# Kernel optimization log

Hardware: AMD Instinct MI355X
Metric: run time of the kernel (lower is better)

Reference implementation:

```python
import jax, jax.numpy as jnp
import numpy as np

K_MASK = -2.3819763e+38
BLOCK_SIZE = 16  # vLLM default paged-KV block size


def apply_rope(inputs, positions, head_dim, max_wavelength=10000):
    # inputs: [B, T, n, H]; positions: [B, T]
    fraction = 2 * jnp.arange(0, head_dim // 2) / head_dim
    timescale = max_wavelength ** fraction
    sinusoid = positions[..., None] / timescale[None, None, :]  # [B, T, H/2]
    sinusoid = sinusoid[..., None, :]                           # [B, T, 1, H/2]
    sin, cos = jnp.sin(sinusoid), jnp.cos(sinusoid)
    first, second = jnp.split(inputs, 2, axis=-1)
    out = jnp.concatenate([first * cos - second * sin,
                           second * cos + first * sin], axis=-1)
    return out.astype(inputs.dtype)


def write_to_cache(proj, cache_side, slot_mapping):
    # proj: [B, T, K, H]; cache_side: [num_slots, K, H]; slot_mapping: [B, T]
    B, T, K, H = proj.shape
    return cache_side.at[slot_mapping.reshape(-1)].set(proj.reshape(B * T, K, H))


def paged_attn(q, k_cache, v_cache, block_tables, context_lens, sm_scale):
    # q: [B, T=1, N, H]; k_cache/v_cache: [num_slots, Kv, H]
    B, T, N, H = q.shape
    Kv = k_cache.shape[1]
    G = N // Kv  # GQA group size
    nb = block_tables.shape[1]
    L = nb * BLOCK_SIZE
    # flat slot indices for every (possibly padded) position of each sequence
    slots = (block_tables[:, :, None] * BLOCK_SIZE
             + jnp.arange(BLOCK_SIZE)[None, None, :]).reshape(B, L)
    keys = k_cache[slots]  # [B, L, Kv, H] gather over non-contiguous blocks
    vals = v_cache[slots]
    qg = q.reshape(B, T, Kv, G, H) * sm_scale
    logits = jnp.einsum('btkgh,blkh->btkgl', qg, keys)
    valid = jnp.arange(L)[None, :] < context_lens[:, None]  # [B, L]
    logits = jnp.where(valid[:, None, None, None, :], logits, K_MASK)
    probs = jax.nn.softmax(logits, axis=-1).astype(keys.dtype)
    out = jnp.einsum('btkgl,blkh->btkgh', probs, vals)
    return out.reshape(B, T, N, H)


def setup_inputs() -> dict:
    key = jax.random.key(0)
    ks = jax.random.split(key, 8)
    B, D, N, Kv, H = 64, 4096, 32, 8, 128
    blocks_per_seq = 64
    num_blocks = B * blocks_per_seq
    num_slots = num_blocks * BLOCK_SIZE  # 65536

    x = jax.random.normal(ks[0], (B, 1, D), jnp.float32)
    context_lens = jax.random.randint(
        ks[1], (B,), 512, blocks_per_seq * BLOCK_SIZE + 1).astype(jnp.int32)
    segment_pos = (context_lens - 1)[:, None].astype(jnp.int32)  # current token pos
    # disjoint block tables: a permutation of all blocks
    block_tables = jax.random.permutation(ks[2], num_blocks).reshape(
        B, blocks_per_seq).astype(jnp.int32)
    last = context_lens - 1
    slot_mapping = (block_tables[jnp.arange(B), last // BLOCK_SIZE] * BLOCK_SIZE
                    + last % BLOCK_SIZE)[:, None].astype(jnp.int32)
    cache = jax.random.normal(ks[3], (2, num_slots, Kv, H), jnp.float32) * 0.02
    q_w = jax.random.normal(ks[4], (N, D, H), jnp.float32) * 0.02
    kv_w = jax.random.normal(ks[5], (2, Kv, D, H), jnp.float32) * 0.02
    o_w = jax.random.normal(ks[6], (N, H, D), jnp.float32) * 0.02
    return dict(x=x, segment_pos=segment_pos, slot_mapping=slot_mapping,
                block_tables=block_tables, context_lens=context_lens,
                cache=cache, q_w=q_w, kv_w=kv_w, o_w=o_w)


def reference(x, segment_pos, slot_mapping, block_tables, context_lens,
              cache, q_w, kv_w, o_w):
    head_dim = q_w.shape[-1]
    sm_scale = head_dim ** (-0.5)
    # GQA projections (num_kv_heads != num_heads path)
    query = jnp.einsum('BTD,NDH->BTNH', x, q_w)
    key_p, val_p = jnp.einsum('BSD,CKDH->CBSKH', x, kv_w)
    query = apply_rope(query, segment_pos, head_dim)
    key_p = apply_rope(key_p, segment_pos, head_dim)
    # scatter-write new K/V into paged cache
    k_cache = write_to_cache(key_p, cache[0], slot_mapping)
    v_cache = write_to_cache(val_p, cache[1], slot_mapping)
    new_cache = jnp.stack([k_cache, v_cache])
    # paged attention over non-contiguous blocks
    out = paged_attn(query, k_cache, v_cache, block_tables, context_lens, sm_scale)
    attn_output = jnp.einsum('BTNH,NHD->BTD', out, o_w)
    return (new_cache, attn_output)
```

## Files before the change

kernel.cpp:

```cpp
#include <hip/hip_runtime.h>
#include <math.h>

#define BB     64
#define DD     4096
#define NQ     32
#define KVH    8
#define GG     4
#define HD     128
#define PAGES  64
#define PSIZE  16
#define NSLOTS 65536
#define CACHE1 67108864UL
#define CACHE2 134217728UL
#define ATTN_ELEMS (BB*DD)
#define K_MASK_F (-2.3819763e+38f)
#define SM_SCALE 0.08838834764831845f

#define WS_QKV 0UL
#define WS_QR  393216UL
#define WS_AT  655360UL
#define WS_KV  917504UL
#define WS_KV_V 65536UL

__global__ __launch_bounds__(256) void kz_zero(float4* __restrict__ ws,
                                               float4* __restrict__ out) {
    const int i = blockIdx.x * 256 + threadIdx.x;
    if (i < 98304) {
        ws[i] = float4{0.f, 0.f, 0.f, 0.f};
    } else {
        out[CACHE2 / 4 + (i - 98304)] = float4{0.f, 0.f, 0.f, 0.f};
    }
}

__global__ __launch_bounds__(256) void k2_qkv(const float* __restrict__ x,
                                              const float* __restrict__ q_w,
                                              const float* __restrict__ kv_w,
                                              float* __restrict__ ws_qkv) {
    const int jt = blockIdx.x;
    const int u  = blockIdx.y;
    const float* w = (u < 32) ? (q_w + (size_t)u * DD * HD)
                              : (kv_w + (size_t)(u - 32) * DD * HD);
    const int t  = threadIdx.x;
    const int dc = t & 31;
    const int bh = t >> 5;

    __shared__ float lx[64][128];
    float acc[8][4];
    #pragma unroll
    for (int i = 0; i < 8; ++i)
        #pragma unroll
        for (int d = 0; d < 4; ++d) acc[i][d] = 0.f;

    for (int chunk = 0; chunk < 4; ++chunk) {
        const int jc = jt * 512 + chunk * 128;
        __syncthreads();
        const float4* x4 = reinterpret_cast<const float4*>(x);
        float4* lx4 = reinterpret_cast<float4*>(&lx[0][0]);
        for (int f = t; f < 64 * 32; f += 256) {
            int i = f >> 5, j4 = f & 31;
            lx4[i * 32 + j4] = x4[(size_t)i * (DD / 4) + (jc / 4) + j4];
        }
        __syncthreads();

        const float* wp = w + (size_t)jc * HD + dc;
        for (int jj4 = 0; jj4 < 32; ++jj4) {
            float wv[4][4];
            #pragma unroll
            for (int q = 0; q < 4; ++q)
                #pragma unroll
                for (int d = 0; d < 4; ++d)
                    wv[q][d] = wp[(size_t)(jj4 * 4 + q) * HD + d * 32];
            #pragma unroll
            for (int i = 0; i < 8; ++i) {
                float4 xv = *reinterpret_cast<const float4*>(&lx[bh * 8 + i][jj4 * 4]);
                #pragma unroll
                for (int d = 0; d < 4; ++d)
                    acc[i][d] += xv.x * wv[0][d] + xv.y * wv[1][d] +
                                 xv.z * wv[2][d] + xv.w * wv[3][d];
            }
        }
    }
    #pragma unroll
    for (int i = 0; i < 8; ++i) {
        int b = bh * 8 + i;
        #pragma unroll
        for (int d = 0; d < 4; ++d)
            atomicAdd(&ws_qkv[((size_t)b * 48 + u) * HD + dc + d * 32], acc[i][d]);
    }
}

__global__ __launch_bounds__(256) void k3_rope(const float* __restrict__ ws_qkv,
                                               float* __restrict__ ws_qr,
                                               float* __restrict__ ws_kv,
                                               const int* __restrict__ segpos) {
    const int b = blockIdx.x;
    const int t = threadIdx.x;
    const float pos = (float)segpos[b];
    const float* qk = ws_qkv + (size_t)b * 48 * 128;

    for (int f = t; f < NQ * 64; f += 256) {
        int n = f >> 6, i = f & 63;
        float ts = __powf(10000.f, (float)i * (1.f / 64.f));
        float ang = pos / ts;
        float s, c;
        sincosf(ang, &s, &c);
        float a = qk[n * 128 + i], d2 = qk[n * 128 + i + 64];
        ws_qr[((size_t)b * NQ + n) * HD + i]      = a * c - d2 * s;
        ws_qr[((size_t)b * NQ + n) * HD + i + 64] = d2 * c + a * s;
    }
    for (int f = t; f < KVH * 64; f += 256) {
        int kh = f >> 6, i = f & 63;
        float ts = __powf(10000.f, (float)i * (1.f / 64.f));
        float ang = pos / ts;
        float s, c;
        sincosf(ang, &s, &c);
        float a = qk[(32 + kh) * 128 + i], d2 = qk[(32 + kh) * 128 + i + 64];
        ws_kv[((size_t)b * KVH + kh) * HD + i]      = a * c - d2 * s;
        ws_kv[((size_t)b * KVH + kh) * HD + i + 64] = d2 * c + a * s;
    }
    for (int f = t; f < KVH * HD; f += 256) {
        int kh = f >> 7, h = f & 127;
        ws_kv[WS_KV_V + ((size_t)b * KVH + kh) * HD + h] = qk[(40 + kh) * 128 + h];
    }
}

__global__ __launch_bounds__(256) void k4_fused(const float* __restrict__ cin,
                                                float* __restrict__ outc,
                                                const float* __restrict__ ws,
                                                float* __restrict__ ws_at,
                                                const int* __restrict__ bt,
                                                const int* __restrict__ ctx) {
    const int k = blockIdx.x;
    const int b = blockIdx.y;
    const int t = threadIdx.x;
    const int Lb = ctx[b];
    const int last = Lb - 1;
    const int npages = (Lb + 15) >> 4;
    const int Lpad = npages << 4;

    __shared__ float logit[GG][PAGES * PSIZE];
    __shared__ float red[4][GG][HD];
    __shared__ float inv_s[GG];

    const int sub = t & 15, pin = t >> 4;
    const int w = t >> 6, lane = t & 63;
    const int* btb = bt + b * PAGES;

    const float* qr = ws + WS_QR + ((size_t)b * NQ + k * GG) * HD;
    float qf[GG][8];
    #pragma unroll
    for (int g = 0; g < GG; ++g) {
        const float4* qp = reinterpret_cast<const float4*>(qr + g * HD + sub * 8);
        float4 q0 = qp[0], q1 = qp[1];
        qf[g][0] = q0.x * SM_SCALE; qf[g][1] = q0.y * SM_SCALE;
        qf[g][2] = q0.z * SM_SCALE; qf[g][3] = q0.w * SM_SCALE;
        qf[g][4] = q1.x * SM_SCALE; qf[g][5] = q1.y * SM_SCALE;
        qf[g][6] = q1.z * SM_SCALE; qf[g][7] = q1.w * SM_SCALE;
    }

    const float* nkp = ws + WS_KV + ((size_t)b * KVH + k) * HD + sub * 8;
    const float4 nk0 = reinterpret_cast<const float4*>(nkp)[0];
    const float4 nk1 = reinterpret_cast<const float4*>(nkp)[1];
    const float4 nv0 = reinterpret_cast<const float4*>(nkp + WS_KV_V)[0];
    const float4 nv1 = reinterpret_cast<const float4*>(nkp + WS_KV_V)[1];

    {
        size_t off = ((size_t)(btb[0] * PSIZE + pin) * KVH + k) * HD + sub * 8;
        float4 a0 = reinterpret_cast<const float4*>(cin + off)[0];
        float4 a1 = reinterpret_cast<const float4*>(cin + off)[1];
        for (int p = 0; p < PAGES; ++p) {
            size_t offn = off;
            float4 b0 = a0, b1 = a1;
            if (p + 1 < PAGES) {
                offn = ((size_t)(btb[p + 1] * PSIZE + pin) * KVH + k) * HD + sub * 8;
                b0 = reinterpret_cast<const float4*>(cin + offn)[0];
                b1 = reinterpret_cast<const float4*>(cin + offn)[1];
            }
            const int gp = (p << 4) + pin;
            if (gp == last) { a0 = nk0; a1 = nk1; }
            reinterpret_cast<float4*>(outc + off)[0] = a0;
            reinterpret_cast<float4*>(outc + off)[1] = a1;
            if (p < npages) {
                #pragma unroll
                for (int g = 0; g < GG; ++g) {
                    float pr = qf[g][0] * a0.x + qf[g][1] * a0.y +
                               qf[g][2] * a0.z + qf[g][3] * a0.w +
                               qf[g][4] * a1.x + qf[g][5] * a1.y +
                               qf[g][6] * a1.z + qf[g][7] * a1.w;
                    #pragma unroll
                    for (int m = 1; m < 16; m <<= 1) pr += __shfl_xor(pr, m);
                    if (sub == 0) logit[g][gp] = (gp < Lb) ? pr : K_MASK_F;
                }
            }
            off = offn; a0 = b0; a1 = b1;
        }
    }
    __syncthreads();

    {
        float m = -INFINITY;
        for (int p = lane; p < Lpad; p += 64) m = fmaxf(m, logit[w][p]);
        #pragma unroll
        for (int s = 1; s < 64; s <<= 1) m = fmaxf(m, __shfl_xor(m, s));
        float sum = 0.f;
        for (int p = lane; p < Lpad; p += 64) {
            float e = __expf(logit[w][p] - m);
            logit[w][p] = e;
            sum += e;
        }
        #pragma unroll
        for (int s = 1; s < 64; s <<= 1) sum += __shfl_xor(sum, s);
        if (lane == 0) inv_s[w] = 1.f / sum;
    }
    __syncthreads();

    float acc[GG][8];
    #pragma unroll
    for (int g = 0; g < GG; ++g)
        #pragma unroll
        for (int j = 0; j < 8; ++j) acc[g][j] = 0.f;
    {
        size_t off = CACHE1 + ((size_t)(btb[0] * PSIZE + pin) * KVH + k) * HD + sub * 8;
        float4 a0 = reinterpret_cast<const float4*>(cin + off)[0];
        float4 a1 = reinterpret_cast<const float4*>(cin + off)[1];
        for (int p = 0; p < PAGES; ++p) {
            size_t offn = off;
            float4 b0 = a0, b1 = a1;
            if (p + 1 < PAGES) {
                offn = CACHE1 + ((size_t)(btb[p + 1] * PSIZE + pin) * KVH + k) * HD + sub * 8;
                b0 = reinterpret_cast<const float4*>(cin + offn)[0];
                b1 = reinterpret_cast<const float4*>(cin + offn)[1];
            }
            const int gp = (p << 4) + pin;
            if (gp == last) { a0 = nv0; a1 = nv1; }
            reinterpret_cast<float4*>(outc + off)[0] = a0;
            reinterpret_cast<float4*>(outc + off)[1] = a1;
            if (p < npages) {
                #pragma unroll
                for (int g = 0; g < GG; ++g) {
                    float e = logit[g][gp];
                    acc[g][0] += e * a0.x; acc[g][1] += e * a0.y;
                    acc[g][2] += e * a0.z; acc[g][3] += e * a0.w;
                    acc[g][4] += e * a1.x; acc[g][5] += e * a1.y;
                    acc[g][6] += e * a1.z; acc[g][7] += e * a1.w;
                }
            }
            off = offn; a0 = b0; a1 = b1;
        }
    }
    #pragma unroll
    for (int g = 0; g < GG; ++g)
        #pragma unroll
        for (int j = 0; j < 8; ++j) {
            acc[g][j] += __shfl_xor(acc[g][j], 16);
            acc[g][j] += __shfl_xor(acc[g][j], 32);
        }
    if (lane < 16) {
        #pragma unroll
        for (int g = 0; g < GG; ++g)
            #pragma unroll
            for (int j = 0; j < 8; ++j) red[w][g][sub * 8 + j] = acc[g][j];
    }
    __syncthreads();

    for (int f = t; f < GG * HD; f += 256) {
        int g = f >> 7, h = f & 127;
        float o = (red[0][g][h] + red[1][g][h] + red[2][g][h] + red[3][g][h]) * inv_s[g];
        ws_at[((size_t)b * NQ + k * GG + g) * HD + h] = o;
    }
}

__global__ __launch_bounds__(256) void k5_oproj(const float* __restrict__ ws,
                                                const float* __restrict__ o_w,
                                                float* __restrict__ out) {
    const int jt = blockIdx.x;
    const int dt = blockIdx.y;
    const int t  = threadIdx.x;
    const int dc = t & 31;
    const int bh = t >> 5;
    const int d0 = dt * 128;

    __shared__ float lx[64][128];
    float acc[8][4];
    #pragma unroll
    for (int i = 0; i < 8; ++i)
        #pragma unroll
        for (int d = 0; d < 4; ++d) acc[i][d] = 0.f;

    const float* xa = ws + WS_AT;
    for (int chunk = 0; chunk < 4; ++chunk) {
        const int jc = jt * 512 + chunk * 128;
        __syncthreads();
        const float4* x4 = reinterpret_cast<const float4*>(xa);
        float4* lx4 = reinterpret_cast<float4*>(&lx[0][0]);
        for (int f = t; f < 64 * 32; f += 256) {
            int i = f >> 5, j4 = f & 31;
            lx4[i * 32 + j4] = x4[(size_t)i * (DD / 4) + (jc / 4) + j4];
        }
        __syncthreads();

        const float* wp = o_w + (size_t)jc * DD + d0 + dc;
        for (int jj4 = 0; jj4 < 32; ++jj4) {
            float wv[4][4];
            #pragma unroll
            for (int q = 0; q < 4; ++q)
                #pragma unroll
                for (int d = 0; d < 4; ++d)
                    wv[q][d] = wp[(size_t)(jj4 * 4 + q) * DD + d * 32];
            #pragma unroll
            for (int i = 0; i < 8; ++i) {
                float4 xv = *reinterpret_cast<const float4*>(&lx[bh * 8 + i][jj4 * 4]);
                #pragma unroll
                for (int d = 0; d < 4; ++d)
                    acc[i][d] += xv.x * wv[0][d] + xv.y * wv[1][d] +
                                 xv.z * wv[2][d] + xv.w * wv[3][d];
            }
        }
    }
    #pragma unroll
    for (int i = 0; i < 8; ++i) {
        int b = bh * 8 + i;
        #pragma unroll
        for (int d = 0; d < 4; ++d)
            atomicAdd(&out[CACHE2 + (size_t)b * DD + d0 + dc + d * 32], acc[i][d]);
    }
}

extern "C" void kernel_launch(void* const* d_in, const int* in_sizes, int n_in,
                              void* d_out, int out_size, void* d_ws, size_t ws_size,
                              hipStream_t stream) {
    const float* x        = (const float*)d_in[0];
    const int*   segpos   = (const int*)d_in[1];
    const int*   slotmap  = (const int*)d_in[2];
    const int*   bt       = (const int*)d_in[3];
    const int*   ctx      = (const int*)d_in[4];
    const float* cache    = (const float*)d_in[5];
    const float* q_w      = (const float*)d_in[6];
    const float* kv_w     = (const float*)d_in[7];
    const float* o_w      = (const float*)d_in[8];
    (void)slotmap;
    float* out = (float*)d_out;
    float* ws  = (float*)d_ws;

    kz_zero<<<640, 256, 0, stream>>>((float4*)ws, (float4*)out);
    k2_qkv<<<dim3(8, 48), 256, 0, stream>>>(x, q_w, kv_w, ws + WS_QKV);
    k3_rope<<<BB, 256, 0, stream>>>(ws + WS_QKV, ws + WS_QR, ws + WS_KV, segpos);
    k4_fused<<<dim3(KVH, BB), 256, 0, stream>>>(cache, out, ws, ws + WS_AT, bt, ctx);
    k5_oproj<<<dim3(8, 32), 256, 0, stream>>>(ws, o_w, out);
}
```

Baseline: 1.149 ms.

## Split GEMM output columns across more blocks, prefetch weights, use nontemporal cache streaming

```diff
diff --git a/kernel.cpp b/kernel.cpp
--- a/kernel.cpp
+++ b/kernel.cpp
@@ -12,7 +12,6 @@
 #define NSLOTS 65536
 #define CACHE1 67108864UL
 #define CACHE2 134217728UL
-#define ATTN_ELEMS (BB*DD)
 #define K_MASK_F (-2.3819763e+38f)
 #define SM_SCALE 0.08838834764831845f
 
@@ -21,6 +20,8 @@
 #define WS_AT  655360UL
 #define WS_KV  917504UL
 #define WS_KV_V 65536UL
+
+typedef float f4v __attribute__((ext_vector_type(4)));
 
 __global__ __launch_bounds__(256) void kz_zero(float4* __restrict__ ws,
                                                float4* __restrict__ out) {
@@ -36,8 +37,9 @@
                                               const float* __restrict__ q_w,
                                               const float* __restrict__ kv_w,
                                               float* __restrict__ ws_qkv) {
-    const int jt = blockIdx.x;
-    const int u  = blockIdx.y;
+    const int jt   = blockIdx.x;
+    const int u    = blockIdx.y >> 1;
+    const int half = (blockIdx.y & 1) * 64;
     const float* w = (u < 32) ? (q_w + (size_t)u * DD * HD)
                               : (kv_w + (size_t)(u - 32) * DD * HD);
     const int t  = threadIdx.x;
@@ -45,11 +47,9 @@
     const int bh = t >> 5;
 
     __shared__ float lx[64][128];
-    float acc[8][4];
-    #pragma unroll
-    for (int i = 0; i < 8; ++i)
-        #pragma unroll
-        for (int d = 0; d < 4; ++d) acc[i][d] = 0.f;
+    float acc[8][2];
+    #pragma unroll
+    for (int i = 0; i < 8; ++i) { acc[i][0] = 0.f; acc[i][1] = 0.f; }
 
     for (int chunk = 0; chunk < 4; ++chunk) {
         const int jc = jt * 512 + chunk * 128;
@@ -62,30 +62,44 @@
         }
         __syncthreads();
 
-        const float* wp = w + (size_t)jc * HD + dc;
+        const float* wp = w + (size_t)jc * HD + half + dc;
+        float wv[4][2];
+        #pragma unroll
+        for (int q = 0; q < 4; ++q)
+            #pragma unroll
+            for (int d = 0; d < 2; ++d) wv[q][d] = wp[(size_t)q * HD + d * 32];
+
         for (int jj4 = 0; jj4 < 32; ++jj4) {
-            float wv[4][4];
-            #pragma unroll
-            for (int q = 0; q < 4; ++q)
-                #pragma unroll
-                for (int d = 0; d < 4; ++d)
-                    wv[q][d] = wp[(size_t)(jj4 * 4 + q) * HD + d * 32];
+            float wn[4][2];
+            if (jj4 < 31) {
+                const float* wpn = wp + (size_t)((jj4 + 1) * 4) * HD;
+                #pragma unroll
+                for (int q = 0; q < 4; ++q)
+                    #pragma unroll
+                    for (int d = 0; d < 2; ++d) wn[q][d] = wpn[(size_t)q * HD + d * 32];
+            }
             #pragma unroll
             for (int i = 0; i < 8; ++i) {
                 float4 xv = *reinterpret_cast<const float4*>(&lx[bh * 8 + i][jj4 * 4]);
                 #pragma unroll
-                for (int d = 0; d < 4; ++d)
+                for (int d = 0; d < 2; ++d)
                     acc[i][d] += xv.x * wv[0][d] + xv.y * wv[1][d] +
                                  xv.z * wv[2][d] + xv.w * wv[3][d];
             }
+            if (jj4 < 31) {
+                #pragma unroll
+                for (int q = 0; q < 4; ++q)
+                    #pragma unroll
+                    for (int d = 0; d < 2; ++d) wv[q][d] = wn[q][d];
+            }
         }
     }
     #pragma unroll
     for (int i = 0; i < 8; ++i) {
         int b = bh * 8 + i;
         #pragma unroll
-        for (int d = 0; d < 4; ++d)
-            atomicAdd(&ws_qkv[((size_t)b * 48 + u) * HD + dc + d * 32], acc[i][d]);
+        for (int d = 0; d < 2; ++d)
+            atomicAdd(&ws_qkv[((size_t)b * 48 + u) * HD + half + dc + d * 32], acc[i][d]);
     }
 }
 
@@ -159,27 +173,19 @@
     }
 
     const float* nkp = ws + WS_KV + ((size_t)b * KVH + k) * HD + sub * 8;
-    const float4 nk0 = reinterpret_cast<const float4*>(nkp)[0];
-    const float4 nk1 = reinterpret_cast<const float4*>(nkp)[1];
-    const float4 nv0 = reinterpret_cast<const float4*>(nkp + WS_KV_V)[0];
-    const float4 nv1 = reinterpret_cast<const float4*>(nkp + WS_KV_V)[1];
 
     {
-        size_t off = ((size_t)(btb[0] * PSIZE + pin) * KVH + k) * HD + sub * 8;
-        float4 a0 = reinterpret_cast<const float4*>(cin + off)[0];
-        float4 a1 = reinterpret_cast<const float4*>(cin + off)[1];
-        for (int p = 0; p < PAGES; ++p) {
-            size_t offn = off;
-            float4 b0 = a0, b1 = a1;
-            if (p + 1 < PAGES) {
-                offn = ((size_t)(btb[p + 1] * PSIZE + pin) * KVH + k) * HD + sub * 8;
-                b0 = reinterpret_cast<const float4*>(cin + offn)[0];
-                b1 = reinterpret_cast<const float4*>(cin + offn)[1];
-            }
+        const f4v nk0 = reinterpret_cast<const f4v*>(nkp)[0];
+        const f4v nk1 = reinterpret_cast<const f4v*>(nkp)[1];
+
+        auto kaddr = [&](int p) -> size_t {
+            return ((size_t)(btb[p] * PSIZE + pin) * KVH + k) * HD + sub * 8;
+        };
+        auto kstep = [&](int p, size_t off, f4v a0, f4v a1) {
             const int gp = (p << 4) + pin;
             if (gp == last) { a0 = nk0; a1 = nk1; }
-            reinterpret_cast<float4*>(outc + off)[0] = a0;
-            reinterpret_cast<float4*>(outc + off)[1] = a1;
+            __builtin_nontemporal_store(a0, reinterpret_cast<f4v*>(outc + off));
+            __builtin_nontemporal_store(a1, reinterpret_cast<f4v*>(outc + off) + 1);
             if (p < npages) {
                 #pragma unroll
                 for (int g = 0; g < GG; ++g) {
@@ -192,7 +198,25 @@
                     if (sub == 0) logit[g][gp] = (gp < Lb) ? pr : K_MASK_F;
                 }
             }
-            off = offn; a0 = b0; a1 = b1;
+        };
+
+        size_t o0 = kaddr(0), o1 = kaddr(1);
+        f4v a00 = __builtin_nontemporal_load(reinterpret_cast<const f4v*>(cin + o0));
+        f4v a01 = __builtin_nontemporal_load(reinterpret_cast<const f4v*>(cin + o0) + 1);
+        f4v a10 = __builtin_nontemporal_load(reinterpret_cast<const f4v*>(cin + o1));
+        f4v a11 = __builtin_nontemporal_load(reinterpret_cast<const f4v*>(cin + o1) + 1);
+        for (int j = 0; j < PAGES / 2; ++j) {
+            const int p = 2 * j;
+            const int pn = (p + 2 < PAGES) ? p + 2 : 0;
+            size_t o2 = kaddr(pn), o3 = kaddr(pn + 1);
+            f4v b00 = __builtin_nontemporal_load(reinterpret_cast<const f4v*>(cin + o2));
+            f4v b01 = __builtin_nontemporal_load(reinterpret_cast<const f4v*>(cin + o2) + 1);
+            f4v b10 = __builtin_nontemporal_load(reinterpret_cast<const f4v*>(cin + o3));
+            f4v b11 = __builtin_nontemporal_load(reinterpret_cast<const f4v*>(cin + o3) + 1);
+            kstep(p, o0, a00, a01);
+            kstep(p + 1, o1, a10, a11);
+            o0 = o2; o1 = o3;
+            a00 = b00; a01 = b01; a10 = b10; a11 = b11;
         }
     }
     __syncthreads();
@@ -220,21 +244,17 @@
         #pragma unroll
         for (int j = 0; j < 8; ++j) acc[g][j] = 0.f;
     {
-        size_t off = CACHE1 + ((size_t)(btb[0] * PSIZE + pin) * KVH + k) * HD + sub * 8;
-        float4 a0 = reinterpret_cast<const float4*>(cin + off)[0];
-        float4 a1 = reinterpret_cast<const float4*>(cin + off)[1];
-        for (int p = 0; p < PAGES; ++p) {
-            size_t offn = off;
-            float4 b0 = a0, b1 = a1;
-            if (p + 1 < PAGES) {
-                offn = CACHE1 + ((size_t)(btb[p + 1] * PSIZE + pin) * KVH + k) * HD + sub * 8;
-                b0 = reinterpret_cast<const float4*>(cin + offn)[0];
-                b1 = reinterpret_cast<const float4*>(cin + offn)[1];
-            }
+        const f4v nv0 = reinterpret_cast<const f4v*>(nkp + WS_KV_V)[0];
+        const f4v nv1 = reinterpret_cast<const f4v*>(nkp + WS_KV_V)[1];
+
+        auto vaddr = [&](int p) -> size_t {
+            return CACHE1 + ((size_t)(btb[p] * PSIZE + pin) * KVH + k) * HD + sub * 8;
+        };
+        auto vstep = [&](int p, size_t off, f4v a0, f4v a1) {
             const int gp = (p << 4) + pin;
             if (gp == last) { a0 = nv0; a1 = nv1; }
-            reinterpret_cast<float4*>(outc + off)[0] = a0;
-            reinterpret_cast<float4*>(outc + off)[1] = a1;
+            __builtin_nontemporal_store(a0, reinterpret_cast<f4v*>(outc + off));
+            __builtin_nontemporal_store(a1, reinterpret_cast<f4v*>(outc + off) + 1);
             if (p < npages) {
                 #pragma unroll
                 for (int g = 0; g < GG; ++g) {
@@ -245,7 +265,25 @@
                     acc[g][6] += e * a1.z; acc[g][7] += e * a1.w;
                 }
             }
-            off = offn; a0 = b0; a1 = b1;
+        };
+
+        size_t o0 = vaddr(0), o1 = vaddr(1);
+        f4v a00 = __builtin_nontemporal_load(reinterpret_cast<const f4v*>(cin + o0));
+        f4v a01 = __builtin_nontemporal_load(reinterpret_cast<const f4v*>(cin + o0) + 1);
+        f4v a10 = __builtin_nontemporal_load(reinterpret_cast<const f4v*>(cin + o1));
+        f4v a11 = __builtin_nontemporal_load(reinterpret_cast<const f4v*>(cin + o1) + 1);
+        for (int j = 0; j < PAGES / 2; ++j) {
+            const int p = 2 * j;
+            const int pn = (p + 2 < PAGES) ? p + 2 : 0;
+            size_t o2 = vaddr(pn), o3 = vaddr(pn + 1);
+            f4v b00 = __builtin_nontemporal_load(reinterpret_cast<const f4v*>(cin + o2));
+            f4v b01 = __builtin_nontemporal_load(reinterpret_cast<const f4v*>(cin + o2) + 1);
+            f4v b10 = __builtin_nontemporal_load(reinterpret_cast<const f4v*>(cin + o3));
+            f4v b11 = __builtin_nontemporal_load(reinterpret_cast<const f4v*>(cin + o3) + 1);
+            vstep(p, o0, a00, a01);
+            vstep(p + 1, o1, a10, a11);
+            o0 = o2; o1 = o3;
+            a00 = b00; a01 = b01; a10 = b10; a11 = b11;
         }
     }
     #pragma unroll
@@ -278,14 +316,12 @@
     const int t  = threadIdx.x;
     const int dc = t & 31;
     const int bh = t >> 5;
-    const int d0 = dt * 128;
+    const int d0 = dt * 64;
 
     __shared__ float lx[64][128];
-    float acc[8][4];
-    #pragma unroll
-    for (int i = 0; i < 8; ++i)
-        #pragma unroll
-        for (int d = 0; d < 4; ++d) acc[i][d] = 0.f;
+    float acc[8][2];
+    #pragma unroll
+    for (int i = 0; i < 8; ++i) { acc[i][0] = 0.f; acc[i][1] = 0.f; }
 
     const float* xa = ws + WS_AT;
     for (int chunk = 0; chunk < 4; ++chunk) {
@@ -300,28 +336,42 @@
         __syncthreads();
 
         const float* wp = o_w + (size_t)jc * DD + d0 + dc;
+        float wv[4][2];
+        #pragma unroll
+        for (int q = 0; q < 4; ++q)
+            #pragma unroll
+            for (int d = 0; d < 2; ++d) wv[q][d] = wp[(size_t)q * DD + d * 32];
+
         for (int jj4 = 0; jj4 < 32; ++jj4) {
-            float wv[4][4];
-            #pragma unroll
-            for (int q = 0; q < 4; ++q)
-                #pragma unroll
-                for (int d = 0; d < 4; ++d)
-                    wv[q][d] = wp[(size_t)(jj4 * 4 + q) * DD + d * 32];
+            float wn[4][2];
+            if (jj4 < 31) {
+                const float* wpn = wp + (size_t)((jj4 + 1) * 4) * DD;
+                #pragma unroll
+                for (int q = 0; q < 4; ++q)
+                    #pragma unroll
+                    for (int d = 0; d < 2; ++d) wn[q][d] = wpn[(size_t)q * DD + d * 32];
+            }
             #pragma unroll
             for (int i = 0; i < 8; ++i) {
                 float4 xv = *reinterpret_cast<const float4*>(&lx[bh * 8 + i][jj4 * 4]);
                 #pragma unroll
-                for (int d = 0; d < 4; ++d)
+                for (int d = 0; d < 2; ++d)
                     acc[i][d] += xv.x * wv[0][d] + xv.y * wv[1][d] +
                                  xv.z * wv[2][d] + xv.w * wv[3][d];
             }
+            if (jj4 < 31) {
+                #pragma unroll
+                for (int q = 0; q < 4; ++q)
+                    #pragma unroll
+                    for (int d = 0; d < 2; ++d) wv[q][d] = wn[q][d];
+            }
         }
     }
     #pragma unroll
     for (int i = 0; i < 8; ++i) {
         int b = bh * 8 + i;
         #pragma unroll
-        for (int d = 0; d < 4; ++d)
+        for (int d = 0; d < 2; ++d)
             atomicAdd(&out[CACHE2 + (size_t)b * DD + d0 + dc + d * 32], acc[i][d]);
     }
 }
@@ -343,8 +393,8 @@
     float* ws  = (float*)d_ws;
 
     kz_zero<<<640, 256, 0, stream>>>((float4*)ws, (float4*)out);
-    k2_qkv<<<dim3(8, 48), 256, 0, stream>>>(x, q_w, kv_w, ws + WS_QKV);
+    k2_qkv<<<dim3(8, 96), 256, 0, stream>>>(x, q_w, kv_w, ws + WS_QKV);
     k3_rope<<<BB, 256, 0, stream>>>(ws + WS_QKV, ws + WS_QR, ws + WS_KV, segpos);
     k4_fused<<<dim3(KVH, BB), 256, 0, stream>>>(cache, out, ws, ws + WS_AT, bt, ctx);
-    k5_oproj<<<dim3(8, 32), 256, 0, stream>>>(ws, o_w, out);
-}
+    k5_oproj<<<dim3(8, 64), 256, 0, stream>>>(ws, o_w, out);
+}
```

Result: faster. 1.120 ms (-2.5%).
